# Kernel tuning notes

Measured on AMD Instinct MI355X. Metric: run time of the kernel, lower is better.

Reference implementation:

```python
import jax, jax.numpy as jnp
import numpy as np
import math

D_MODEL = 1024
D_STATE = 16
D_CONV = 4
EXPAND = 2
D_INNER = EXPAND * D_MODEL          # 2048
DT_RANK = math.ceil(D_MODEL / 16)    # 64
B_SZ, T_LEN = 2, 1024
DT_MIN, DT_MAX, DT_FLOOR = 1e-3, 1e-1, 1e-4


def setup_inputs() -> dict:
    key = jax.random.key(0)
    ks = jax.random.split(key, 10)
    s = 0.02
    x = jax.random.normal(ks[0], (B_SZ, T_LEN, D_MODEL), jnp.float32)
    W_in = jax.random.normal(ks[1], (2 * D_INNER, D_MODEL), jnp.float32) * s
    conv_w = jax.random.normal(ks[2], (D_INNER, 1, D_CONV), jnp.float32) * 0.2  # depthwise (O,1,K)
    conv_b = jax.random.normal(ks[3], (D_INNER,), jnp.float32) * 0.02
    W_x = jax.random.normal(ks[4], (DT_RANK + 2 * D_STATE, D_INNER), jnp.float32) * s
    dt_std = DT_RANK ** -0.5
    W_dt = jax.random.uniform(ks[5], (D_INNER, DT_RANK), jnp.float32, -dt_std, dt_std)
    dt = jnp.exp(jax.random.uniform(ks[6], (D_INNER,), jnp.float32)
                 * (math.log(DT_MAX) - math.log(DT_MIN)) + math.log(DT_MIN))
    dt = jnp.clip(dt, DT_FLOOR, None)
    b_dt = dt + jnp.log(-jnp.expm1(-dt))  # inverse-softplus init
    A_log = jnp.log(jnp.broadcast_to(jnp.arange(1, D_STATE + 1, dtype=jnp.float32),
                                     (D_INNER, D_STATE)))
    D_param = jnp.ones((D_INNER,), jnp.float32)
    W_out = jax.random.normal(ks[7], (D_MODEL, D_INNER), jnp.float32) * s
    return {"x": x, "W_in": W_in, "conv_w": conv_w, "conv_b": conv_b,
            "W_x": W_x, "W_dt": W_dt, "b_dt": b_dt, "A_log": A_log,
            "D_param": D_param, "W_out": W_out}


def reference(x, W_in, conv_w, conv_b, W_x, W_dt, b_dt, A_log, D_param, W_out):
    silu = jax.nn.silu
    # input projection -> (B,T,2*D_INNER), split into x_inner / gate z
    xz = jnp.einsum('btd,ed->bte', x, W_in)
    x_inner, z = xz[..., :D_INNER], xz[..., D_INNER:]
    # depthwise causal conv1d: left-pad K-1 (== torch pad both + slice [:T])
    xc = jnp.transpose(x_inner, (0, 2, 1))  # (B, D_INNER, T)
    xc = jax.lax.conv_general_dilated(
        xc, conv_w, window_strides=(1,), padding=[(D_CONV - 1, 0)],
        feature_group_count=D_INNER,
        dimension_numbers=('NCH', 'OIH', 'NCH')) + conv_b[None, :, None]
    x_conv = jnp.transpose(silu(xc), (0, 2, 1))  # (B,T,D_INNER)
    # SSM parameter projections
    x_dbl = jnp.einsum('btd,ed->bte', x_conv, W_x)
    dt_low = x_dbl[..., :DT_RANK]
    B_ssm = x_dbl[..., DT_RANK:DT_RANK + D_STATE]          # (B,T,N)
    C_ssm = x_dbl[..., DT_RANK + D_STATE:]                 # (B,T,N)
    dt = jax.nn.softplus(jnp.einsum('btr,dr->btd', dt_low, W_dt) + b_dt)
    A = -jnp.exp(A_log)                                    # (D_INNER, N)
    # discretize: h_t = dA_t * h_{t-1} + dBx_t, h_{-1} = 0
    dA = jnp.exp(dt[..., None] * A)                        # (B,T,D,N)
    dBx = dt[..., None] * B_ssm[:, :, None, :] * x_conv[..., None]
    def comb(c1, c2):
        a1, b1 = c1
        a2, b2 = c2
        return a1 * a2, a2 * b1 + b2
    _, h = jax.lax.associative_scan(comb, (dA, dBx), axis=1)  # (B,T,D,N)
    y = jnp.einsum('btdn,btn->btd', h, C_ssm)
    y = y * silu(z) + D_param * x_conv
    out = jnp.einsum('btd,ed->bte', y, W_out)
    return out
```

## Files before the change

kernel.cpp:

```cpp
#include <hip/hip_runtime.h>
#include <cstdint>

#define D_MODEL 1024
#define D_STATE 16
#define D_INNER 2048
#define DT_RANK 64
#define BSZ 2
#define TLEN 1024
#define M_TOK (BSZ*TLEN)
#define NXZ (2*D_INNER)
#define NXDBL 128
#define TC 16
#define NCHUNK (TLEN/TC)

typedef unsigned short u16;
typedef short s16x8 __attribute__((ext_vector_type(8)));
typedef float f32x4 __attribute__((ext_vector_type(4)));

__device__ __forceinline__ u16 f2bf(float f) {
  uint32_t u = __float_as_uint(f);
  u += 0x7fffu + ((u >> 16) & 1u);
  return (u16)(u >> 16);
}
__device__ __forceinline__ float bf2f(u16 u) {
  return __uint_as_float(((uint32_t)u) << 16);
}

#define GLDS16(g, l) __builtin_amdgcn_global_load_lds( \
    (const __attribute__((address_space(1))) void*)(g), \
    (__attribute__((address_space(3))) void*)(l), 16, 0, 0)

__global__ __launch_bounds__(256) void cvt_all(
    const float* __restrict__ s0, u16* __restrict__ d0, int n0,
    const float* __restrict__ s1, u16* __restrict__ d1, int n1,
    const float* __restrict__ s2, u16* __restrict__ d2, int n2,
    const float* __restrict__ s3, u16* __restrict__ d3, int n3)
{
  int total = n0 + n1 + n2 + n3;
  for (int i = blockIdx.x*256 + threadIdx.x; i < total; i += gridDim.x*256) {
    const float* s; u16* d; int j = i;
    if (j < n0)            { s = s0; d = d0; }
    else if ((j -= n0) < n1) { s = s1; d = d1; }
    else if ((j -= n1) < n2) { s = s2; d = d2; }
    else                   { j -= n2; s = s3; d = d3; }
    float4 v = ((const float4*)s)[j];
    u16* dst = d + (size_t)j*4;
    dst[0] = f2bf(v.x); dst[1] = f2bf(v.y); dst[2] = f2bf(v.z); dst[3] = f2bf(v.w);
  }
}

__global__ __launch_bounds__(256) void wx_pad(const float* __restrict__ wx, u16* __restrict__ dst)
{
  int i = blockIdx.x*256 + threadIdx.x;
  int row = i >> 9;
  u16* d = dst + (size_t)i*4;
  if (row < 96) {
    float4 v = ((const float4*)wx)[i];
    d[0] = f2bf(v.x); d[1] = f2bf(v.y); d[2] = f2bf(v.z); d[3] = f2bf(v.w);
  } else {
    d[0] = 0; d[1] = 0; d[2] = 0; d[3] = 0;
  }
}

template<int EPI, int FM, int FN, int OBF>
__global__ __launch_bounds__(256) void gemm_bt(
    const u16* __restrict__ A, const u16* __restrict__ B,
    void* __restrict__ Cv, int M, int N, int K,
    const float* __restrict__ bias, int kchunk)
{
  constexpr int BMt = FM*32;
  constexpr int BNt = FN*32;
  constexpr int AOPS = BMt/16;
  constexpr int TOPS = (BMt+BNt)/16;
  constexpr int NOPS = TOPS/4;
  __shared__ __align__(16) u16 As[BMt*32];
  __shared__ __align__(16) u16 Bs[BNt*32];
  const int tid  = threadIdx.x;
  const int lane = tid & 63;
  const int wv   = tid >> 6;
  const int m0 = blockIdx.x * BMt;
  const int n0 = blockIdx.y * BNt;
  const int kb = blockIdx.z * kchunk;
  const int ke = kb + kchunk;
  const int wr = wv >> 1, wc = wv & 1;

  f32x4 acc[FM][FN];
#pragma unroll
  for (int i = 0; i < FM; i++)
#pragma unroll
    for (int j = 0; j < FN; j++) acc[i][j] = (f32x4){0.f,0.f,0.f,0.f};

  const int rl = lane >> 2;
  const int c8 = (lane & 3) * 8;
  const u16* srcs[NOPS];
  u16* dsts[NOPS];
#pragma unroll
  for (int t = 0; t < NOPS; t++) {
    int op = wv + t*4;
    if (op < AOPS) {
      srcs[t] = A + (size_t)(m0 + op*16 + rl)*K + c8;
      dsts[t] = &As[op*512];
    } else {
      srcs[t] = B + (size_t)(n0 + (op-AOPS)*16 + rl)*K + c8;
      dsts[t] = &Bs[(op-AOPS)*512];
    }
  }

  const int fr = lane & 15;
  const int ko = (lane >> 4) * 8;
  for (int k0 = kb; k0 < ke; k0 += 32) {
    __syncthreads();
#pragma unroll
    for (int t = 0; t < NOPS; t++) GLDS16(srcs[t] + k0, dsts[t]);
    __syncthreads();
    s16x8 af[FM], bfv[FN];
#pragma unroll
    for (int i = 0; i < FM; i++) af[i]  = *(const s16x8*)&As[(wr*FM*16 + i*16 + fr)*32 + ko];
#pragma unroll
    for (int j = 0; j < FN; j++) bfv[j] = *(const s16x8*)&Bs[(wc*FN*16 + j*16 + fr)*32 + ko];
#pragma unroll
    for (int i = 0; i < FM; i++)
#pragma unroll
      for (int j = 0; j < FN; j++)
        acc[i][j] = __builtin_amdgcn_mfma_f32_16x16x32_bf16(af[i], bfv[j], acc[i][j], 0, 0, 0);
  }

  float* Cf = (float*)Cv + (size_t)blockIdx.z * M * N;
  u16*   Ch = (u16*)Cv;
  const int cr = (lane >> 4) * 4;
  const int cc = lane & 15;
#pragma unroll
  for (int i = 0; i < FM; i++) {
#pragma unroll
    for (int j = 0; j < FN; j++) {
      const int col = n0 + (wc*FN + j)*16 + cc;
      float bv = (EPI == 1) ? bias[col] : 0.f;
#pragma unroll
      for (int q = 0; q < 4; q++) {
        const int row = m0 + (wr*FM + i)*16 + cr + q;
        float v = acc[i][j][q];
        if (EPI == 1) { v += bv; v = (v > 20.f) ? v : log1pf(__expf(v)); }
        if (OBF) Ch[(size_t)row*N + col] = f2bf(v);
        else     Cf[(size_t)row*N + col] = v;
      }
    }
  }
}

__global__ __launch_bounds__(256) void conv_silu(
    const u16* __restrict__ xz, const float* __restrict__ cw,
    const float* __restrict__ cb, u16* __restrict__ xcb)
{
  int j = blockIdx.x*256 + threadIdx.x;
  int d0 = (j & 511) * 4;
  int m = j >> 9;
  int t = m & (TLEN-1);
  const float4* cwp = (const float4*)(cw + (size_t)d0*4);
  float4 wr0 = cwp[0], wr1 = cwp[1], wr2 = cwp[2], wr3 = cwp[3];
  const float w0[4] = {wr0.x, wr0.y, wr0.z, wr0.w};
  const float w1[4] = {wr1.x, wr1.y, wr1.z, wr1.w};
  const float w2[4] = {wr2.x, wr2.y, wr2.z, wr2.w};
  const float w3[4] = {wr3.x, wr3.y, wr3.z, wr3.w};
  float4 acc = *(const float4*)(cb + d0);
#pragma unroll
  for (int jj = 0; jj < 4; jj++) {
    int tt = t - 3 + jj;
    if (tt >= 0) {
      union { uint2 v; u16 u[4]; } ld;
      ld.v = *(const uint2*)(xz + (size_t)(m-3+jj)*NXZ + d0);
      acc.x = fmaf(w0[jj], bf2f(ld.u[0]), acc.x);
      acc.y = fmaf(w1[jj], bf2f(ld.u[1]), acc.y);
      acc.z = fmaf(w2[jj], bf2f(ld.u[2]), acc.z);
      acc.w = fmaf(w3[jj], bf2f(ld.u[3]), acc.w);
    }
  }
  float4 r;
  r.x = acc.x / (1.f + __expf(-acc.x));
  r.y = acc.y / (1.f + __expf(-acc.y));
  r.z = acc.z / (1.f + __expf(-acc.z));
  r.w = acc.w / (1.f + __expf(-acc.w));
  union { u16 u[4]; uint2 v; } o;
  o.u[0] = f2bf(r.x); o.u[1] = f2bf(r.y); o.u[2] = f2bf(r.z); o.u[3] = f2bf(r.w);
  *(uint2*)(xcb + (size_t)m*D_INNER + d0) = o.v;
}

__global__ __launch_bounds__(256) void prep(
    const float* __restrict__ part, float* __restrict__ xdbl, u16* __restrict__ dtl)
{
  int idx = blockIdx.x*256 + threadIdx.x;
  float s = 0.f;
#pragma unroll
  for (int c = 0; c < 8; c++) s += part[(size_t)c*M_TOK*NXDBL + idx];
  xdbl[idx] = s;
  int col = idx & 127;
  if (col < DT_RANK) {
    int m = idx >> 7;
    dtl[(size_t)m*DT_RANK + col] = f2bf(s);
  }
}

__global__ __launch_bounds__(256) void scan1(
    const u16* __restrict__ dt, const u16* __restrict__ xc,
    const float* __restrict__ xdbl, const float* __restrict__ A_log,
    float* __restrict__ P, float* __restrict__ S)
{
  const int bid = blockIdx.x;
  const int dblk = bid & 7;
  const int b = (bid >> 3) & 1;
  const int chunk = bid >> 4;
  const int d = dblk*256 + threadIdx.x;

  float Ac[16];
  {
    const float4* Ap = (const float4*)(A_log + (size_t)d*D_STATE);
#pragma unroll
    for (int q = 0; q < 4; q++) {
      float4 v = Ap[q];
      Ac[q*4+0] = -__expf(v.x); Ac[q*4+1] = -__expf(v.y);
      Ac[q*4+2] = -__expf(v.z); Ac[q*4+3] = -__expf(v.w);
    }
  }
  float h[16], p[16];
#pragma unroll
  for (int n = 0; n < 16; n++) { h[n] = 0.f; p[n] = 1.f; }

  const int m0 = b*TLEN + chunk*TC;
  for (int i = 0; i < TC; i++) {
    const size_t m = m0 + i;
    float dtv = bf2f(dt[m*D_INNER + d]);
    float xv  = bf2f(xc[m*D_INNER + d]);
    float dbx = dtv * xv;
    const float4* Bp = (const float4*)(xdbl + m*NXDBL + DT_RANK);
    float4 B0 = Bp[0], B1 = Bp[1], B2 = Bp[2], B3 = Bp[3];
    float Bv[16] = {B0.x,B0.y,B0.z,B0.w, B1.x,B1.y,B1.z,B1.w,
                    B2.x,B2.y,B2.z,B2.w, B3.x,B3.y,B3.z,B3.w};
#pragma unroll
    for (int n = 0; n < 16; n++) {
      float dA = __expf(dtv * Ac[n]);
      h[n] = fmaf(dA, h[n], dbx * Bv[n]);
      p[n] *= dA;
    }
  }
  size_t o = ((size_t)((chunk*2 + b)*D_INNER + d))*D_STATE;
  float4* Pp = (float4*)(P + o);
  float4* Sp = (float4*)(S + o);
#pragma unroll
  for (int q = 0; q < 4; q++) {
    Pp[q] = (float4){p[q*4+0], p[q*4+1], p[q*4+2], p[q*4+3]};
    Sp[q] = (float4){h[q*4+0], h[q*4+1], h[q*4+2], h[q*4+3]};
  }
}

__global__ __launch_bounds__(256) void stitch(
    const float* __restrict__ P, float* __restrict__ S)
{
  int idx = blockIdx.x*256 + threadIdx.x;
  const size_t stride = 2*D_INNER*D_STATE;
  float h = 0.f;
#pragma unroll 4
  for (int c = 0; c < NCHUNK; c++) {
    size_t o = (size_t)c*stride + idx;
    float p = P[o], s = S[o];
    S[o] = h;
    h = fmaf(p, h, s);
  }
}

__global__ __launch_bounds__(256) void scan2(
    const u16* __restrict__ dt, const u16* __restrict__ xc,
    const float* __restrict__ xdbl, const float* __restrict__ A_log,
    const float* __restrict__ Hpref, const u16* __restrict__ xz,
    const float* __restrict__ Dp, u16* __restrict__ yb)
{
  const int bid = blockIdx.x;
  const int dblk = bid & 7;
  const int b = (bid >> 3) & 1;
  const int chunk = bid >> 4;
  const int d = dblk*256 + threadIdx.x;

  float Ac[16];
  {
    const float4* Ap = (const float4*)(A_log + (size_t)d*D_STATE);
#pragma unroll
    for (int q = 0; q < 4; q++) {
      float4 v = Ap[q];
      Ac[q*4+0] = -__expf(v.x); Ac[q*4+1] = -__expf(v.y);
      Ac[q*4+2] = -__expf(v.z); Ac[q*4+3] = -__expf(v.w);
    }
  }
  float h[16];
  {
    size_t o = ((size_t)((chunk*2 + b)*D_INNER + d))*D_STATE;
    const float4* Hp = (const float4*)(Hpref + o);
#pragma unroll
    for (int q = 0; q < 4; q++) {
      float4 v = Hp[q];
      h[q*4+0] = v.x; h[q*4+1] = v.y; h[q*4+2] = v.z; h[q*4+3] = v.w;
    }
  }
  const float Dv = Dp[d];
  const int m0 = b*TLEN + chunk*TC;
  for (int i = 0; i < TC; i++) {
    const size_t m = m0 + i;
    float dtv = bf2f(dt[m*D_INNER + d]);
    float xv  = bf2f(xc[m*D_INNER + d]);
    float dbx = dtv * xv;
    const float4* Bp = (const float4*)(xdbl + m*NXDBL + DT_RANK);
    float4 B0 = Bp[0], B1 = Bp[1], B2 = Bp[2], B3 = Bp[3];
    const float4* Cp = (const float4*)(xdbl + m*NXDBL + DT_RANK + D_STATE);
    float4 C0 = Cp[0], C1 = Cp[1], C2 = Cp[2], C3 = Cp[3];
    float Bv[16] = {B0.x,B0.y,B0.z,B0.w, B1.x,B1.y,B1.z,B1.w,
                    B2.x,B2.y,B2.z,B2.w, B3.x,B3.y,B3.z,B3.w};
    float Cv[16] = {C0.x,C0.y,C0.z,C0.w, C1.x,C1.y,C1.z,C1.w,
                    C2.x,C2.y,C2.z,C2.w, C3.x,C3.y,C3.z,C3.w};
    float y = 0.f;
#pragma unroll
    for (int n = 0; n < 16; n++) {
      float dA = __expf(dtv * Ac[n]);
      h[n] = fmaf(dA, h[n], dbx * Bv[n]);
      y = fmaf(h[n], Cv[n], y);
    }
    float z = bf2f(xz[m*NXZ + D_INNER + d]);
    float sz = z/(1.f + __expf(-z));
    yb[m*D_INNER + d] = f2bf(fmaf(y, sz, Dv*xv));
  }
}

extern "C" void kernel_launch(void* const* d_in, const int* in_sizes, int n_in,
                              void* d_out, int out_size, void* d_ws, size_t ws_size,
                              hipStream_t stream)
{
  const float* x     = (const float*)d_in[0];
  const float* W_in  = (const float*)d_in[1];
  const float* convw = (const float*)d_in[2];
  const float* convb = (const float*)d_in[3];
  const float* W_x   = (const float*)d_in[4];
  const float* W_dt  = (const float*)d_in[5];
  const float* b_dt  = (const float*)d_in[6];
  const float* A_log = (const float*)d_in[7];
  const float* Dp    = (const float*)d_in[8];
  const float* W_out = (const float*)d_in[9];
  float* out = (float*)d_out;

  char* w = (char*)d_ws;
  size_t o = 0;
  auto alloc = [&](size_t bytes) { char* p = w + o; o = (o + bytes + 255) & ~(size_t)255; return p; };
  u16*   xb   = (u16*)  alloc((size_t)M_TOK*D_MODEL*2);
  u16*   Wib  = (u16*)  alloc((size_t)NXZ*D_MODEL*2);
  u16*   Wxb  = (u16*)  alloc((size_t)NXDBL*D_INNER*2);
  u16*   Wdtb = (u16*)  alloc((size_t)D_INNER*DT_RANK*2);
  u16*   Wob  = (u16*)  alloc((size_t)D_MODEL*D_INNER*2);
  u16*   xzb  = (u16*)  alloc((size_t)M_TOK*NXZ*2);
  u16*   xcb  = (u16*)  alloc((size_t)M_TOK*D_INNER*2);
  float* part = (float*)alloc((size_t)8*M_TOK*NXDBL*4);
  float* xdbl = (float*)alloc((size_t)M_TOK*NXDBL*4);
  u16*   dtl  = (u16*)  alloc((size_t)M_TOK*DT_RANK*2);
  u16*   dtb  = (u16*)  alloc((size_t)M_TOK*D_INNER*2);
  float* Pb   = (float*)alloc((size_t)NCHUNK*2*D_INNER*D_STATE*4);
  float* Sb   = (float*)alloc((size_t)NCHUNK*2*D_INNER*D_STATE*4);
  u16*   yb   = (u16*)  alloc((size_t)M_TOK*D_INNER*2);
  (void)ws_size; (void)n_in; (void)in_sizes; (void)out_size;

  cvt_all<<<2048,256,0,stream>>>(x, xb, (M_TOK*D_MODEL)/4,
                                 W_in, Wib, (NXZ*D_MODEL)/4,
                                 W_dt, Wdtb, (D_INNER*DT_RANK)/4,
                                 W_out, Wob, (D_MODEL*D_INNER)/4);
  wx_pad<<<(NXDBL*D_INNER/4)/256,256,0,stream>>>(W_x, Wxb);
  gemm_bt<0,2,4,1><<<dim3(M_TOK/64, NXZ/128, 1),256,0,stream>>>(xb, Wib, xzb, M_TOK, NXZ, D_MODEL, nullptr, D_MODEL);
  conv_silu<<<(M_TOK*D_INNER/4)/256,256,0,stream>>>(xzb, convw, convb, xcb);
  gemm_bt<0,2,2,0><<<dim3(M_TOK/64, NXDBL/64, 8),256,0,stream>>>(xcb, Wxb, part, M_TOK, NXDBL, D_INNER, nullptr, D_INNER/8);
  prep<<<(M_TOK*NXDBL)/256,256,0,stream>>>(part, xdbl, dtl);
  gemm_bt<1,2,2,1><<<dim3(M_TOK/64, D_INNER/64, 1),256,0,stream>>>(dtl, Wdtb, dtb, M_TOK, D_INNER, DT_RANK, b_dt, DT_RANK);
  scan1<<<8*2*NCHUNK,256,0,stream>>>(dtb, xcb, xdbl, A_log, Pb, Sb);
  stitch<<<(2*D_INNER*D_STATE)/256,256,0,stream>>>(Pb, Sb);
  scan2<<<8*2*NCHUNK,256,0,stream>>>(dtb, xcb, xdbl, A_log, Sb, xzb, Dp, yb);
  gemm_bt<0,2,2,0><<<dim3(M_TOK/64, D_MODEL/64, 1),256,0,stream>>>(yb, Wob, out, M_TOK, D_MODEL, D_INNER, nullptr, D_INNER);
}
```

Baseline: 252.3 us.

## Stage SSM B/C in shared memory, compact B/C buffer, fold W_x pad into convert

```diff
diff --git a/kernel.cpp b/kernel.cpp
--- a/kernel.cpp
+++ b/kernel.cpp
@@ -34,31 +34,23 @@
     const float* __restrict__ s0, u16* __restrict__ d0, int n0,
     const float* __restrict__ s1, u16* __restrict__ d1, int n1,
     const float* __restrict__ s2, u16* __restrict__ d2, int n2,
-    const float* __restrict__ s3, u16* __restrict__ d3, int n3)
-{
-  int total = n0 + n1 + n2 + n3;
+    const float* __restrict__ s3, u16* __restrict__ d3, int n3,
+    const float* __restrict__ s4, u16* __restrict__ d4, int n4)
+{
+  int total = n0 + n1 + n2 + n3 + n4;
   for (int i = blockIdx.x*256 + threadIdx.x; i < total; i += gridDim.x*256) {
-    const float* s; u16* d; int j = i;
-    if (j < n0)            { s = s0; d = d0; }
+    const float* s; u16* d; int j = i; bool pad = false;
+    if (j < n0)              { s = s0; d = d0; }
     else if ((j -= n0) < n1) { s = s1; d = d1; }
     else if ((j -= n1) < n2) { s = s2; d = d2; }
-    else                   { j -= n2; s = s3; d = d3; }
-    float4 v = ((const float4*)s)[j];
+    else if ((j -= n2) < n3) { s = s3; d = d3; }
+    else { j -= n3; s = s4; d = d4; pad = ((j >> 9) >= 96); }
     u16* dst = d + (size_t)j*4;
-    dst[0] = f2bf(v.x); dst[1] = f2bf(v.y); dst[2] = f2bf(v.z); dst[3] = f2bf(v.w);
-  }
-}
-
-__global__ __launch_bounds__(256) void wx_pad(const float* __restrict__ wx, u16* __restrict__ dst)
-{
-  int i = blockIdx.x*256 + threadIdx.x;
-  int row = i >> 9;
-  u16* d = dst + (size_t)i*4;
-  if (row < 96) {
-    float4 v = ((const float4*)wx)[i];
-    d[0] = f2bf(v.x); d[1] = f2bf(v.y); d[2] = f2bf(v.z); d[3] = f2bf(v.w);
-  } else {
-    d[0] = 0; d[1] = 0; d[2] = 0; d[3] = 0;
+    if (pad) { dst[0] = 0; dst[1] = 0; dst[2] = 0; dst[3] = 0; }
+    else {
+      float4 v = ((const float4*)s)[j];
+      dst[0] = f2bf(v.x); dst[1] = f2bf(v.y); dst[2] = f2bf(v.z); dst[3] = f2bf(v.w);
+    }
   }
 }
 
@@ -185,30 +177,36 @@
 }
 
 __global__ __launch_bounds__(256) void prep(
-    const float* __restrict__ part, float* __restrict__ xdbl, u16* __restrict__ dtl)
+    const float* __restrict__ part, float* __restrict__ bc, u16* __restrict__ dtl)
 {
   int idx = blockIdx.x*256 + threadIdx.x;
+  int col = idx & 127;
+  if (col >= DT_RANK + 2*D_STATE) return;
   float s = 0.f;
 #pragma unroll
   for (int c = 0; c < 8; c++) s += part[(size_t)c*M_TOK*NXDBL + idx];
-  xdbl[idx] = s;
-  int col = idx & 127;
-  if (col < DT_RANK) {
-    int m = idx >> 7;
-    dtl[(size_t)m*DT_RANK + col] = f2bf(s);
-  }
+  int m = idx >> 7;
+  if (col < DT_RANK) dtl[(size_t)m*DT_RANK + col] = f2bf(s);
+  else               bc[(size_t)m*32 + (col - DT_RANK)] = s;
 }
 
 __global__ __launch_bounds__(256) void scan1(
     const u16* __restrict__ dt, const u16* __restrict__ xc,
-    const float* __restrict__ xdbl, const float* __restrict__ A_log,
+    const float* __restrict__ bc, const float* __restrict__ A_log,
     float* __restrict__ P, float* __restrict__ S)
 {
+  __shared__ float Bsh[TC*16];
   const int bid = blockIdx.x;
   const int dblk = bid & 7;
   const int b = (bid >> 3) & 1;
   const int chunk = bid >> 4;
   const int d = dblk*256 + threadIdx.x;
+  const int m0 = b*TLEN + chunk*TC;
+
+  {
+    int r = threadIdx.x;
+    Bsh[r] = bc[(size_t)(m0 + (r >> 4))*32 + (r & 15)];
+  }
 
   float Ac[16];
   {
@@ -223,21 +221,17 @@
   float h[16], p[16];
 #pragma unroll
   for (int n = 0; n < 16; n++) { h[n] = 0.f; p[n] = 1.f; }
-
-  const int m0 = b*TLEN + chunk*TC;
+  __syncthreads();
+
   for (int i = 0; i < TC; i++) {
     const size_t m = m0 + i;
     float dtv = bf2f(dt[m*D_INNER + d]);
     float xv  = bf2f(xc[m*D_INNER + d]);
     float dbx = dtv * xv;
-    const float4* Bp = (const float4*)(xdbl + m*NXDBL + DT_RANK);
-    float4 B0 = Bp[0], B1 = Bp[1], B2 = Bp[2], B3 = Bp[3];
-    float Bv[16] = {B0.x,B0.y,B0.z,B0.w, B1.x,B1.y,B1.z,B1.w,
-                    B2.x,B2.y,B2.z,B2.w, B3.x,B3.y,B3.z,B3.w};
 #pragma unroll
     for (int n = 0; n < 16; n++) {
       float dA = __expf(dtv * Ac[n]);
-      h[n] = fmaf(dA, h[n], dbx * Bv[n]);
+      h[n] = fmaf(dA, h[n], dbx * Bsh[i*16 + n]);
       p[n] *= dA;
     }
   }
@@ -268,15 +262,23 @@
 
 __global__ __launch_bounds__(256) void scan2(
     const u16* __restrict__ dt, const u16* __restrict__ xc,
-    const float* __restrict__ xdbl, const float* __restrict__ A_log,
+    const float* __restrict__ bc, const float* __restrict__ A_log,
     const float* __restrict__ Hpref, const u16* __restrict__ xz,
     const float* __restrict__ Dp, u16* __restrict__ yb)
 {
+  __shared__ float BCsh[TC*32];
   const int bid = blockIdx.x;
   const int dblk = bid & 7;
   const int b = (bid >> 3) & 1;
   const int chunk = bid >> 4;
   const int d = dblk*256 + threadIdx.x;
+  const int m0 = b*TLEN + chunk*TC;
+
+  {
+    int r = threadIdx.x;
+    BCsh[r]       = bc[(size_t)m0*32 + r];
+    BCsh[r + 256] = bc[(size_t)m0*32 + r + 256];
+  }
 
   float Ac[16];
   {
@@ -299,26 +301,19 @@
     }
   }
   const float Dv = Dp[d];
-  const int m0 = b*TLEN + chunk*TC;
+  __syncthreads();
+
   for (int i = 0; i < TC; i++) {
     const size_t m = m0 + i;
     float dtv = bf2f(dt[m*D_INNER + d]);
     float xv  = bf2f(xc[m*D_INNER + d]);
     float dbx = dtv * xv;
-    const float4* Bp = (const float4*)(xdbl + m*NXDBL + DT_RANK);
-    float4 B0 = Bp[0], B1 = Bp[1], B2 = Bp[2], B3 = Bp[3];
-    const float4* Cp = (const float4*)(xdbl + m*NXDBL + DT_RANK + D_STATE);
-    float4 C0 = Cp[0], C1 = Cp[1], C2 = Cp[2], C3 = Cp[3];
-    float Bv[16] = {B0.x,B0.y,B0.z,B0.w, B1.x,B1.y,B1.z,B1.w,
-                    B2.x,B2.y,B2.z,B2.w, B3.x,B3.y,B3.z,B3.w};
-    float Cv[16] = {C0.x,C0.y,C0.z,C0.w, C1.x,C1.y,C1.z,C1.w,
-                    C2.x,C2.y,C2.z,C2.w, C3.x,C3.y,C3.z,C3.w};
     float y = 0.f;
 #pragma unroll
     for (int n = 0; n < 16; n++) {
       float dA = __expf(dtv * Ac[n]);
-      h[n] = fmaf(dA, h[n], dbx * Bv[n]);
-      y = fmaf(h[n], Cv[n], y);
+      h[n] = fmaf(dA, h[n], dbx * BCsh[i*32 + n]);
+      y = fmaf(h[n], BCsh[i*32 + 16 + n], y);
     }
     float z = bf2f(xz[m*NXZ + D_INNER + d]);
     float sz = z/(1.f + __expf(-z));
@@ -353,7 +348,7 @@
   u16*   xzb  = (u16*)  alloc((size_t)M_TOK*NXZ*2);
   u16*   xcb  = (u16*)  alloc((size_t)M_TOK*D_INNER*2);
   float* part = (float*)alloc((size_t)8*M_TOK*NXDBL*4);
-  float* xdbl = (float*)alloc((size_t)M_TOK*NXDBL*4);
+  float* bcb  = (float*)alloc((size_t)M_TOK*32*4);
   u16*   dtl  = (u16*)  alloc((size_t)M_TOK*DT_RANK*2);
   u16*   dtb  = (u16*)  alloc((size_t)M_TOK*D_INNER*2);
   float* Pb   = (float*)alloc((size_t)NCHUNK*2*D_INNER*D_STATE*4);
@@ -364,15 +359,15 @@
   cvt_all<<<2048,256,0,stream>>>(x, xb, (M_TOK*D_MODEL)/4,
                                  W_in, Wib, (NXZ*D_MODEL)/4,
                                  W_dt, Wdtb, (D_INNER*DT_RANK)/4,
-                                 W_out, Wob, (D_MODEL*D_INNER)/4);
-  wx_pad<<<(NXDBL*D_INNER/4)/256,256,0,stream>>>(W_x, Wxb);
+                                 W_out, Wob, (D_MODEL*D_INNER)/4,
+                                 W_x, Wxb, (NXDBL*D_INNER)/4);
   gemm_bt<0,2,4,1><<<dim3(M_TOK/64, NXZ/128, 1),256,0,stream>>>(xb, Wib, xzb, M_TOK, NXZ, D_MODEL, nullptr, D_MODEL);
   conv_silu<<<(M_TOK*D_INNER/4)/256,256,0,stream>>>(xzb, convw, convb, xcb);
   gemm_bt<0,2,2,0><<<dim3(M_TOK/64, NXDBL/64, 8),256,0,stream>>>(xcb, Wxb, part, M_TOK, NXDBL, D_INNER, nullptr, D_INNER/8);
-  prep<<<(M_TOK*NXDBL)/256,256,0,stream>>>(part, xdbl, dtl);
+  prep<<<(M_TOK*NXDBL)/256,256,0,stream>>>(part, bcb, dtl);
   gemm_bt<1,2,2,1><<<dim3(M_TOK/64, D_INNER/64, 1),256,0,stream>>>(dtl, Wdtb, dtb, M_TOK, D_INNER, DT_RANK, b_dt, DT_RANK);
-  scan1<<<8*2*NCHUNK,256,0,stream>>>(dtb, xcb, xdbl, A_log, Pb, Sb);
+  scan1<<<8*2*NCHUNK,256,0,stream>>>(dtb, xcb, bcb, A_log, Pb, Sb);
   stitch<<<(2*D_INNER*D_STATE)/256,256,0,stream>>>(Pb, Sb);
-  scan2<<<8*2*NCHUNK,256,0,stream>>>(dtb, xcb, xdbl, A_log, Sb, xzb, Dp, yb);
+  scan2<<<8*2*NCHUNK,256,0,stream>>>(dtb, xcb, bcb, A_log, Sb, xzb, Dp, yb);
   gemm_bt<0,2,2,0><<<dim3(M_TOK/64, D_MODEL/64, 1),256,0,stream>>>(yb, Wob, out, M_TOK, D_MODEL, D_INNER, nullptr, D_INNER);
 }
```

Result: no change. 248.1 us (-1.7%).
